# Performance work log

Measured on AMD Instinct MI355X. Metric: run time of the kernel, lower is better.

Reference implementation:

```python
import jax, jax.numpy as jnp
import numpy as np

B, L, V, H = 2, 2048, 1024, 16
HD = V // H  # head size 64
EPS = 1e-3   # keras LayerNormalization default


def setup_inputs() -> dict:
    key = jax.random.key(0)
    ks = jax.random.split(key, 10)
    scale = 1.0 / np.sqrt(V)
    return {
        "query": jax.random.normal(ks[0], (B, L, V), jnp.float32),
        "key_t": jax.random.normal(ks[1], (B, L, V), jnp.float32),
        "value": jax.random.normal(ks[2], (B, L, V), jnp.float32),
        "Wq": jax.random.normal(ks[3], (H, V, HD), jnp.float32) * scale,
        "Wk": jax.random.normal(ks[4], (H, V, HD), jnp.float32) * scale,
        "Wv": jax.random.normal(ks[5], (H, V, HD), jnp.float32) * scale,
        "gamma": jnp.ones((V,), jnp.float32),
        "beta": jnp.zeros((V,), jnp.float32),
        "query_mask": jax.random.randint(ks[6], (B, L), 0, 2, jnp.int32),
        "value_mask": jax.random.randint(ks[7], (B, L), 0, 2, jnp.int32),
    }


def reference(query, key_t, value, Wq, Wk, Wv, gamma, beta, query_mask, value_mask):
    qm = query_mask.astype(jnp.float32)  # (B,L)
    vm = value_mask.astype(jnp.float32)  # (B,L)

    # per-head no-bias Dense projections, batched over heads
    Q = jnp.einsum('blv,hvd->bhld', query, Wq)
    K = jnp.einsum('blv,hvd->bhld', key_t, Wk)
    Vh = jnp.einsum('blv,hvd->bhld', value, Wv)

    scores = jnp.einsum('bhld,bhmd->bhlm', Q, K) / jnp.sqrt(jnp.float32(HD))
    attn = jax.nn.softmax(scores, axis=-1)

    # post-softmax multiplicative masking (faithful to original)
    tri = jnp.tril(jnp.ones((L, L), jnp.float32))  # (L,L) causal
    attn = attn * tri[None, None, :, :]
    attn = attn * qm[:, None, :, None] * vm[:, None, None, :]

    heads = jnp.einsum('bhlm,bhmd->bhld', attn, Vh)
    x = heads.transpose(0, 2, 1, 3).reshape(B, L, V)  # concat heads

    # dropout is identity at inference
    y = x + query
    mu = jnp.mean(y, axis=-1, keepdims=True)
    var = jnp.mean((y - mu) ** 2, axis=-1, keepdims=True)
    return gamma * (y - mu) * jax.lax.rsqrt(var + EPS) + beta
```

## Files before the change

kernel.cpp:

```cpp
#include <hip/hip_runtime.h>
#include <math.h>

constexpr int NB = 2;
constexpr int SL = 2048;
constexpr int NV = 1024;
constexpr int NH = 16;
constexpr int DH = 64;
constexpr float LN_EPS = 1e-3f;

typedef __bf16 bf16_t;
typedef __bf16 v8bf __attribute__((ext_vector_type(8)));
typedef float  v4f  __attribute__((ext_vector_type(4)));

__device__ __forceinline__ unsigned pack_bf16(float a, float b) {
  unsigned short ua = __builtin_bit_cast(unsigned short, (bf16_t)a);
  unsigned short ub = __builtin_bit_cast(unsigned short, (bf16_t)b);
  return (unsigned)ua | ((unsigned)ub << 16);
}
__device__ __forceinline__ void async_cp16(const void* g, void* l) {
  __builtin_amdgcn_global_load_lds(
      (const __attribute__((address_space(1))) unsigned int*)g,
      (__attribute__((address_space(3))) unsigned int*)l, 16, 0, 0);
}
__device__ __forceinline__ void drain_dma() {
  asm volatile("s_waitcnt vmcnt(0)" ::: "memory");
}

__global__ __launch_bounds__(256)
void acvt(const float* __restrict__ q, const float* __restrict__ k,
          const float* __restrict__ v, bf16_t* __restrict__ oq,
          bf16_t* __restrict__ ok, bf16_t* __restrict__ ov) {
  const int z = blockIdx.y;
  const float* src = z == 0 ? q : (z == 1 ? k : v);
  bf16_t*      dst = z == 0 ? oq : (z == 1 ? ok : ov);
  const size_t i = ((size_t)blockIdx.x * 256 + threadIdx.x) * 4;
  float4 f = *(const float4*)(src + i);
  uint2 u = {pack_bf16(f.x, f.y), pack_bf16(f.z, f.w)};
  *(uint2*)(dst + i) = u;
}

__global__ __launch_bounds__(256)
void wcvt(const float* __restrict__ Wq, const float* __restrict__ Wk,
          const float* __restrict__ Wv, bf16_t* __restrict__ Wt) {
  __shared__ float ls[64][65];
  const int z = blockIdx.z;
  const float* W = z == 0 ? Wq : (z == 1 ? Wk : Wv);
  const float sc = z == 0 ? 0.125f * 1.44269504f : 1.0f;
  const int h = blockIdx.y, v0 = blockIdx.x * 64;
  const int t = threadIdx.x;
  const int rr = t >> 4, c4 = t & 15;
  const float* src = W + ((size_t)h * NV + v0) * DH;
#pragma unroll
  for (int it = 0; it < 4; ++it) {
    float4 f = *(const float4*)(src + (size_t)(rr + it * 16) * DH + c4 * 4);
    ls[rr + it * 16][c4 * 4 + 0] = f.x;
    ls[rr + it * 16][c4 * 4 + 1] = f.y;
    ls[rr + it * 16][c4 * 4 + 2] = f.z;
    ls[rr + it * 16][c4 * 4 + 3] = f.w;
  }
  __syncthreads();
  const int dd = t >> 2, vq = t & 3;
  bf16_t tmp[16];
#pragma unroll
  for (int i = 0; i < 16; ++i) tmp[i] = (bf16_t)(ls[vq * 16 + i][dd] * sc);
  bf16_t* dst = Wt + ((size_t)z * NV + h * 64 + dd) * NV + v0 + vq * 16;
  *(v8bf*)dst = *(v8bf*)&tmp[0];
  *(v8bf*)(dst + 8) = *(v8bf*)&tmp[8];
}

__global__ __launch_bounds__(256, 4)
void proj_mfma(const bf16_t* __restrict__ A0, const bf16_t* __restrict__ A1,
               const bf16_t* __restrict__ A2, const bf16_t* __restrict__ Wtb,
               const int* __restrict__ vmask,
               bf16_t* __restrict__ O0, bf16_t* __restrict__ O1,
               bf16_t* __restrict__ O2) {
  __shared__ __align__(16) bf16_t Asb[2][128 * 32];
  __shared__ __align__(16) bf16_t Wsb[2][128 * 32];

  const int z = blockIdx.z;
  const bf16_t* A   = z == 0 ? A0 : (z == 1 ? A1 : A2);
  bf16_t*       out = z == 0 ? O0 : (z == 1 ? O1 : O2);
  const bf16_t* W   = Wtb + (size_t)z * NV * NV;

  const int t = threadIdx.x, w = t >> 6, lane = t & 63;
  const int g = lane >> 4, lx = lane & 15;
  const int m0 = blockIdx.x * 128, n0 = blockIdx.y * 128;
  const int rbase = (w >> 1) * 64, cbase = (w & 1) * 64;

  const int sr = lane >> 2;
  const int sc = (lane & 3);
  auto stageA = [&](int k0, int buf) {
#pragma unroll
    for (int s = 0; s < 2; ++s) {
      const int r = w * 32 + s * 16 + sr;
      const int c = sc ^ (r & 3);
      async_cp16(A + (size_t)(m0 + r) * NV + k0 + c * 8,
                 (char*)Asb[buf] + (w * 32 + s * 16) * 64);
    }
  };
  auto stageW = [&](int k0, int buf) {
#pragma unroll
    for (int s = 0; s < 2; ++s) {
      const int r = w * 32 + s * 16 + sr;
      const int c = sc ^ (r & 3);
      async_cp16(W + (size_t)(n0 + r) * NV + k0 + c * 8,
                 (char*)Wsb[buf] + (w * 32 + s * 16) * 64);
    }
  };

  v4f acc[4][4] = {};
  stageA(0, 0);
  stageW(0, 0);

  for (int it = 0; it < 32; ++it) {
    const int buf = it & 1;
    drain_dma();
    __syncthreads();
    if (it < 31) {
      stageA((it + 1) * 32, buf ^ 1);
      stageW((it + 1) * 32, buf ^ 1);
    }
    v8bf af[4], wf[4];
#pragma unroll
    for (int rt = 0; rt < 4; ++rt) {
      const int row = rbase + rt * 16 + lx;
      af[rt] = *(const v8bf*)((const char*)Asb[buf] + row * 64 +
                              ((g ^ (row & 3)) * 16));
    }
#pragma unroll
    for (int ct = 0; ct < 4; ++ct) {
      const int row = cbase + ct * 16 + lx;
      wf[ct] = *(const v8bf*)((const char*)Wsb[buf] + row * 64 +
                              ((g ^ (row & 3)) * 16));
    }
#pragma unroll
    for (int rt = 0; rt < 4; ++rt)
#pragma unroll
      for (int ct = 0; ct < 4; ++ct)
        acc[rt][ct] = __builtin_amdgcn_mfma_f32_16x16x32_bf16(
            af[rt], wf[ct], acc[rt][ct], 0, 0, 0);
  }

  if (z < 2) {
#pragma unroll
    for (int rt = 0; rt < 4; ++rt) {
#pragma unroll
      for (int reg = 0; reg < 4; ++reg) {
        const int row = m0 + rbase + rt * 16 + g * 4 + reg;
        const int b = row >> 11, l = row & (SL - 1);
#pragma unroll
        for (int ct = 0; ct < 4; ++ct) {
          const int n = n0 + cbase + ct * 16 + lx;
          const int h = n >> 6, d = n & 63;
          out[((size_t)(b * NH + h) * SL + l) * DH + d] = (bf16_t)acc[rt][ct][reg];
        }
      }
    }
  } else {
#pragma unroll
    for (int rt = 0; rt < 4; ++rt) {
      const int row = m0 + rbase + rt * 16 + g * 4;
      const int b = row >> 11, l = row & (SL - 1);
      float vm0 = (float)vmask[b * SL + l + 0];
      float vm1 = (float)vmask[b * SL + l + 1];
      float vm2 = (float)vmask[b * SL + l + 2];
      float vm3 = (float)vmask[b * SL + l + 3];
#pragma unroll
      for (int ct = 0; ct < 4; ++ct) {
        const int n = n0 + cbase + ct * 16 + lx;
        const int h = n >> 6, d = n & 63;
        uint2 u = {pack_bf16(acc[rt][ct][0] * vm0, acc[rt][ct][1] * vm1),
                   pack_bf16(acc[rt][ct][2] * vm2, acc[rt][ct][3] * vm3)};
        *(uint2*)&out[((size_t)(b * NH + h) * DH + d) * SL + l] = u;
      }
    }
  }
}

__global__ __launch_bounds__(256, 4)
void attn_mfma(const bf16_t* __restrict__ Qg, const bf16_t* __restrict__ Kg,
               const bf16_t* __restrict__ Vtg_all, const int* __restrict__ qmask,
               float* __restrict__ Xout) {
  __shared__ __align__(16) bf16_t kbuf[2][64 * 64];
  __shared__ __align__(16) bf16_t vbuf[2][64 * 64];
  __shared__ __align__(16) bf16_t Ps[4][32 * 32];

  const int id = blockIdx.x;
  const int bh = (id & 7) | ((id >> 8) << 3);
  const int qraw = (id >> 3) & 31;
  const int qb = ((id >> 8) & 1) ? qraw : 31 - qraw;
  const int t = threadIdx.x, w = t >> 6, lane = t & 63;
  const int wq = w & 1, wm = w >> 1;
  const int g = lane >> 4, lx = lane & 15;
  const int b = bh >> 4, h = bh & 15;
  const int l0 = qb * 64;
  const int lastAct = qb;

  const bf16_t* Kb  = Kg + (size_t)bh * SL * DH;
  const bf16_t* Vtg = Vtg_all + (size_t)bh * DH * SL;

  v8bf qf[2][2];
#pragma unroll
  for (int qt = 0; qt < 2; ++qt)
#pragma unroll
    for (int ks = 0; ks < 2; ++ks)
      qf[qt][ks] = *(const v8bf*)&Qg[((size_t)bh * SL + l0 + wq * 32 + qt * 16 + lx) * DH +
                                     ks * 32 + g * 8];

  v4f O[2][4] = {};
  float suml[2] = {0.f, 0.f};

  const int sr_off = lane >> 3, sc_l = lane & 7;
  auto stageK = [&](int mb, int buf) {
#pragma unroll
    for (int s = 0; s < 2; ++s) {
      const int r = w * 16 + s * 8 + sr_off;
      const int c = sc_l ^ (r & 7);
      async_cp16(Kb + (size_t)(mb + r) * DH + c * 8,
                 (char*)kbuf[buf] + (w * 16 + s * 8) * 128);
    }
  };
  auto stageV = [&](int mb, int buf) {
#pragma unroll
    for (int s = 0; s < 2; ++s) {
      const int r = w * 16 + s * 8 + sr_off;
      const int c = sc_l ^ (r & 7);
      async_cp16(Vtg + (size_t)r * SL + mb + c * 8,
                 (char*)vbuf[buf] + (w * 16 + s * 8) * 128);
    }
  };

  stageK(0, 0);
  stageV(0, 0);

  for (int mt = 0; mt <= lastAct; ++mt) {
    const int pb = mt & 1;
    drain_dma();
    __syncthreads();
    if (mt < SL / 64 - 1)  stageK((mt + 1) * 64, pb ^ 1);
    if (mt + 1 <= lastAct) stageV((mt + 1) * 64, pb ^ 1);

    v4f S[2][2];
#pragma unroll
    for (int mt2 = 0; mt2 < 2; ++mt2) {
      S[mt2][0] = (v4f){0.f, 0.f, 0.f, 0.f};
      S[mt2][1] = (v4f){0.f, 0.f, 0.f, 0.f};
    }
#pragma unroll
    for (int ks = 0; ks < 2; ++ks)
#pragma unroll
      for (int mt2 = 0; mt2 < 2; ++mt2) {
        const int row = wm * 32 + mt2 * 16 + lx;
        v8bf kf = *(const v8bf*)((const char*)kbuf[pb] + row * 128 +
                                 (((ks * 4 + g) ^ (lx & 7)) * 16));
#pragma unroll
        for (int qt = 0; qt < 2; ++qt)
          S[mt2][qt] = __builtin_amdgcn_mfma_f32_16x16x32_bf16(
              kf, qf[qt][ks], S[mt2][qt], 0, 0, 0);
      }

    const bool diagzone = (mt == qb);
#pragma unroll
    for (int mt2 = 0; mt2 < 2; ++mt2)
#pragma unroll
      for (int qt = 0; qt < 2; ++qt) {
        float e0 = __builtin_amdgcn_exp2f(S[mt2][qt][0]);
        float e1 = __builtin_amdgcn_exp2f(S[mt2][qt][1]);
        float e2 = __builtin_amdgcn_exp2f(S[mt2][qt][2]);
        float e3 = __builtin_amdgcn_exp2f(S[mt2][qt][3]);
        suml[qt] += (e0 + e1) + (e2 + e3);
        if (diagzone) {
          const int ml = mt * 64 + wm * 32 + mt2 * 16 + g * 4;
          const int ql = l0 + wq * 32 + qt * 16 + lx;
          e0 = (ml + 0 <= ql) ? e0 : 0.f;
          e1 = (ml + 1 <= ql) ? e1 : 0.f;
          e2 = (ml + 2 <= ql) ? e2 : 0.f;
          e3 = (ml + 3 <= ql) ? e3 : 0.f;
        }
        uint2 u = {pack_bf16(e0, e1), pack_bf16(e2, e3)};
        *(uint2*)((char*)Ps[w] + (qt * 16 + lx) * 64 +
                  (((mt2 * 2 + (g >> 1)) ^ ((lx >> 1) & 3)) * 16) +
                  (g & 1) * 8) = u;
      }

    __builtin_amdgcn_wave_barrier();

    v8bf pf[2];
#pragma unroll
    for (int qt = 0; qt < 2; ++qt)
      pf[qt] = *(const v8bf*)((const char*)Ps[w] + (qt * 16 + lx) * 64 +
                              ((g ^ ((lx >> 1) & 3)) * 16));
#pragma unroll
    for (int dt = 0; dt < 4; ++dt) {
      const int row = dt * 16 + lx;
      v8bf vf = *(const v8bf*)((const char*)vbuf[pb] + row * 128 +
                               (((wm * 4 + g) ^ (lx & 7)) * 16));
#pragma unroll
      for (int qt = 0; qt < 2; ++qt)
        O[qt][dt] = __builtin_amdgcn_mfma_f32_16x16x32_bf16(
            pf[qt], vf, O[qt][dt], 0, 0, 0);
    }
  }

  for (int mt = lastAct + 1; mt < SL / 64; ++mt) {
    const int pb = mt & 1;
    drain_dma();
    __syncthreads();
    if (mt < SL / 64 - 1) stageK((mt + 1) * 64, pb ^ 1);
    v4f S[2][2];
#pragma unroll
    for (int mt2 = 0; mt2 < 2; ++mt2) {
      S[mt2][0] = (v4f){0.f, 0.f, 0.f, 0.f};
      S[mt2][1] = (v4f){0.f, 0.f, 0.f, 0.f};
    }
#pragma unroll
    for (int ks = 0; ks < 2; ++ks)
#pragma unroll
      for (int mt2 = 0; mt2 < 2; ++mt2) {
        const int row = wm * 32 + mt2 * 16 + lx;
        v8bf kf = *(const v8bf*)((const char*)kbuf[pb] + row * 128 +
                                 (((ks * 4 + g) ^ (lx & 7)) * 16));
#pragma unroll
        for (int qt = 0; qt < 2; ++qt)
          S[mt2][qt] = __builtin_amdgcn_mfma_f32_16x16x32_bf16(
              kf, qf[qt][ks], S[mt2][qt], 0, 0, 0);
      }
#pragma unroll
    for (int mt2 = 0; mt2 < 2; ++mt2)
#pragma unroll
      for (int qt = 0; qt < 2; ++qt)
        suml[qt] += (__builtin_amdgcn_exp2f(S[mt2][qt][0]) +
                     __builtin_amdgcn_exp2f(S[mt2][qt][1])) +
                    (__builtin_amdgcn_exp2f(S[mt2][qt][2]) +
                     __builtin_amdgcn_exp2f(S[mt2][qt][3]));
  }

  suml[0] += __shfl_xor(suml[0], 16); suml[0] += __shfl_xor(suml[0], 32);
  suml[1] += __shfl_xor(suml[1], 16); suml[1] += __shfl_xor(suml[1], 32);

  __syncthreads();
  float* obuf = (float*)&kbuf[0][0];
  float* sbuf = (float*)&vbuf[0][0];
  if (g == 0) {
    sbuf[((wq * 2 + wm) * 2 + 0) * 16 + lx] = suml[0];
    sbuf[((wq * 2 + wm) * 2 + 1) * 16 + lx] = suml[1];
  }
  if (wm == 1) {
#pragma unroll
    for (int qt = 0; qt < 2; ++qt)
#pragma unroll
      for (int dt = 0; dt < 4; ++dt)
#pragma unroll
        for (int reg = 0; reg < 4; ++reg)
          obuf[wq * 2048 + (qt * 16 + g * 4 + reg) * 64 +
               ((dt * 16 + lx) ^ ((g & 1) * 16))] = O[qt][dt][reg];
  }
  __syncthreads();
  if (wm == 0) {
#pragma unroll
    for (int qt = 0; qt < 2; ++qt) {
      const float stot = suml[qt] + sbuf[((wq * 2 + 1) * 2 + qt) * 16 + lx];
#pragma unroll
      for (int reg = 0; reg < 4; ++reg) {
        const int q = l0 + wq * 32 + qt * 16 + g * 4 + reg;
        const float den = __shfl(stot, g * 4 + reg);
        const float inv = (float)qmask[b * SL + q] / den;
#pragma unroll
        for (int dt = 0; dt < 4; ++dt) {
          const float val =
              (O[qt][dt][reg] +
               obuf[wq * 2048 + (qt * 16 + g * 4 + reg) * 64 +
                    ((dt * 16 + lx) ^ ((g & 1) * 16))]) *
              inv;
          Xout[((size_t)(b * SL + q)) * NV + h * DH + dt * 16 + lx] = val;
        }
      }
    }
  }
}

__global__ __launch_bounds__(256)
void ln_kernel(const float* __restrict__ X, const float* __restrict__ query,
               const float* __restrict__ gamma, const float* __restrict__ beta,
               float* __restrict__ out) {
  const int row = blockIdx.x * 4 + (threadIdx.x >> 6);
  const int lane = threadIdx.x & 63;
  const float* xr = X + (size_t)row * NV;
  const float* qr = query + (size_t)row * NV;
  float4 y[4];
  float s = 0.f, ss = 0.f;
#pragma unroll
  for (int i = 0; i < 4; ++i) {
    const int col = lane * 4 + i * 256;
    float4 xv = *(const float4*)(xr + col);
    float4 qv = *(const float4*)(qr + col);
    y[i].x = xv.x + qv.x; y[i].y = xv.y + qv.y;
    y[i].z = xv.z + qv.z; y[i].w = xv.w + qv.w;
    s  += (y[i].x + y[i].y) + (y[i].z + y[i].w);
    ss += (y[i].x * y[i].x + y[i].y * y[i].y) +
          (y[i].z * y[i].z + y[i].w * y[i].w);
  }
#pragma unroll
  for (int off = 1; off < 64; off <<= 1) {
    s  += __shfl_xor(s, off);
    ss += __shfl_xor(ss, off);
  }
  const float mu   = s * (1.f / NV);
  const float var  = ss * (1.f / NV) - mu * mu;
  const float rstd = rsqrtf(var + LN_EPS);
#pragma unroll
  for (int i = 0; i < 4; ++i) {
    const int col = lane * 4 + i * 256;
    float4 gv = *(const float4*)(gamma + col);
    float4 bv = *(const float4*)(beta + col);
    float4 o;
    o.x = gv.x * (y[i].x - mu) * rstd + bv.x;
    o.y = gv.y * (y[i].y - mu) * rstd + bv.y;
    o.z = gv.z * (y[i].z - mu) * rstd + bv.z;
    o.w = gv.w * (y[i].w - mu) * rstd + bv.w;
    *(float4*)(out + (size_t)row * NV + col) = o;
  }
}

extern "C" void kernel_launch(void* const* d_in, const int* in_sizes, int n_in,
                              void* d_out, int out_size, void* d_ws, size_t ws_size,
                              hipStream_t stream) {
  const float* query = (const float*)d_in[0];
  const float* key_t = (const float*)d_in[1];
  const float* value = (const float*)d_in[2];
  const float* Wq    = (const float*)d_in[3];
  const float* Wk    = (const float*)d_in[4];
  const float* Wv    = (const float*)d_in[5];
  const float* gamma = (const float*)d_in[6];
  const float* beta  = (const float*)d_in[7];
  const int*   qmask = (const int*)d_in[8];
  const int*   vmask = (const int*)d_in[9];
  float* out = (float*)d_out;

  const size_t per = (size_t)NB * NH * SL * DH;
  bf16_t* Qws = (bf16_t*)d_ws;
  bf16_t* Kws = Qws + per;
  bf16_t* Vws = Kws + per;
  bf16_t* Wtb = Vws + per;
  bf16_t* Aq  = Wtb + (size_t)3 * NV * NV;
  bf16_t* Ak  = Aq + per;
  bf16_t* Av  = Ak + per;

  acvt<<<dim3((NB * SL * NV) / (256 * 4), 3), 256, 0, stream>>>(
      query, key_t, value, Aq, Ak, Av);
  wcvt<<<dim3(16, 16, 3), 256, 0, stream>>>(Wq, Wk, Wv, Wtb);
  proj_mfma<<<dim3(32, 8, 3), 256, 0, stream>>>(Aq, Ak, Av, Wtb,
                                                vmask, Qws, Kws, Vws);
  attn_mfma<<<1024, 256, 0, stream>>>(Qws, Kws, Vws, qmask, out);
  ln_kernel<<<NB * SL / 4, 256, 0, stream>>>(out, query, gamma, beta, out);
}
```

Before: 206.1 us.

## Load K and V fragments directly from global memory instead of LDS staging

Removes the double-buffered async global-to-LDS staging of K and V tiles and the per-iteration drain and block barrier. Each wave now loads its MFMA K and V fragments straight from global memory, and the shared buffer shrinks to hold only the P tiles and the epilogue buffers. This cuts LDS use and synchronisation, which may allow more resident blocks, but it gives up cross-wave reuse of K/V tiles and the prefetch overlap. Global and L2 traffic rises, and load latency is now exposed directly in the inner loop.

```diff
diff --git a/kernel.cpp b/kernel.cpp
--- a/kernel.cpp
+++ b/kernel.cpp
@@ -181,9 +181,10 @@
 void attn_mfma(const bf16_t* __restrict__ Qg, const bf16_t* __restrict__ Kg,
                const bf16_t* __restrict__ Vtg_all, const int* __restrict__ qmask,
                float* __restrict__ Xout) {
-  __shared__ __align__(16) bf16_t kbuf[2][64 * 64];
-  __shared__ __align__(16) bf16_t vbuf[2][64 * 64];
-  __shared__ __align__(16) bf16_t Ps[4][32 * 32];
+  __shared__ __align__(16) char smem[16896];
+  bf16_t* Ps   = (bf16_t*)smem;
+  float*  obuf = (float*)smem;
+  float*  sbuf = (float*)(smem + 16384);
 
   const int id = blockIdx.x;
   const int bh = (id & 7) | ((id >> 8) << 3);
@@ -210,36 +211,8 @@
   v4f O[2][4] = {};
   float suml[2] = {0.f, 0.f};
 
-  const int sr_off = lane >> 3, sc_l = lane & 7;
-  auto stageK = [&](int mb, int buf) {
-#pragma unroll
-    for (int s = 0; s < 2; ++s) {
-      const int r = w * 16 + s * 8 + sr_off;
-      const int c = sc_l ^ (r & 7);
-      async_cp16(Kb + (size_t)(mb + r) * DH + c * 8,
-                 (char*)kbuf[buf] + (w * 16 + s * 8) * 128);
-    }
-  };
-  auto stageV = [&](int mb, int buf) {
-#pragma unroll
-    for (int s = 0; s < 2; ++s) {
-      const int r = w * 16 + s * 8 + sr_off;
-      const int c = sc_l ^ (r & 7);
-      async_cp16(Vtg + (size_t)r * SL + mb + c * 8,
-                 (char*)vbuf[buf] + (w * 16 + s * 8) * 128);
-    }
-  };
-
-  stageK(0, 0);
-  stageV(0, 0);
-
   for (int mt = 0; mt <= lastAct; ++mt) {
-    const int pb = mt & 1;
-    drain_dma();
-    __syncthreads();
-    if (mt < SL / 64 - 1)  stageK((mt + 1) * 64, pb ^ 1);
-    if (mt + 1 <= lastAct) stageV((mt + 1) * 64, pb ^ 1);
-
+    const int mb = mt * 64;
     v4f S[2][2];
 #pragma unroll
     for (int mt2 = 0; mt2 < 2; ++mt2) {
@@ -250,9 +223,8 @@
     for (int ks = 0; ks < 2; ++ks)
 #pragma unroll
       for (int mt2 = 0; mt2 < 2; ++mt2) {
-        const int row = wm * 32 + mt2 * 16 + lx;
-        v8bf kf = *(const v8bf*)((const char*)kbuf[pb] + row * 128 +
-                                 (((ks * 4 + g) ^ (lx & 7)) * 16));
+        v8bf kf = *(const v8bf*)&Kb[(size_t)(mb + wm * 32 + mt2 * 16 + lx) * DH +
+                                    ks * 32 + g * 8];
 #pragma unroll
         for (int qt = 0; qt < 2; ++qt)
           S[mt2][qt] = __builtin_amdgcn_mfma_f32_16x16x32_bf16(
@@ -270,7 +242,7 @@
         float e3 = __builtin_amdgcn_exp2f(S[mt2][qt][3]);
         suml[qt] += (e0 + e1) + (e2 + e3);
         if (diagzone) {
-          const int ml = mt * 64 + wm * 32 + mt2 * 16 + g * 4;
+          const int ml = mb + wm * 32 + mt2 * 16 + g * 4;
           const int ql = l0 + wq * 32 + qt * 16 + lx;
           e0 = (ml + 0 <= ql) ? e0 : 0.f;
           e1 = (ml + 1 <= ql) ? e1 : 0.f;
@@ -278,7 +250,7 @@
           e3 = (ml + 3 <= ql) ? e3 : 0.f;
         }
         uint2 u = {pack_bf16(e0, e1), pack_bf16(e2, e3)};
-        *(uint2*)((char*)Ps[w] + (qt * 16 + lx) * 64 +
+        *(uint2*)((char*)&Ps[w * 1024] + (qt * 16 + lx) * 64 +
                   (((mt2 * 2 + (g >> 1)) ^ ((lx >> 1) & 3)) * 16) +
                   (g & 1) * 8) = u;
       }
@@ -288,13 +260,12 @@
     v8bf pf[2];
 #pragma unroll
     for (int qt = 0; qt < 2; ++qt)
-      pf[qt] = *(const v8bf*)((const char*)Ps[w] + (qt * 16 + lx) * 64 +
+      pf[qt] = *(const v8bf*)((const char*)&Ps[w * 1024] + (qt * 16 + lx) * 64 +
                               ((g ^ ((lx >> 1) & 3)) * 16));
 #pragma unroll
     for (int dt = 0; dt < 4; ++dt) {
-      const int row = dt * 16 + lx;
-      v8bf vf = *(const v8bf*)((const char*)vbuf[pb] + row * 128 +
-                               (((wm * 4 + g) ^ (lx & 7)) * 16));
+      v8bf vf = *(const v8bf*)&Vtg[(size_t)(dt * 16 + lx) * SL + mb +
+                                   wm * 32 + g * 8];
 #pragma unroll
       for (int qt = 0; qt < 2; ++qt)
         O[qt][dt] = __builtin_amdgcn_mfma_f32_16x16x32_bf16(
@@ -303,10 +274,7 @@
   }
 
   for (int mt = lastAct + 1; mt < SL / 64; ++mt) {
-    const int pb = mt & 1;
-    drain_dma();
-    __syncthreads();
-    if (mt < SL / 64 - 1) stageK((mt + 1) * 64, pb ^ 1);
+    const int mb = mt * 64;
     v4f S[2][2];
 #pragma unroll
     for (int mt2 = 0; mt2 < 2; ++mt2) {
@@ -317,9 +285,8 @@
     for (int ks = 0; ks < 2; ++ks)
 #pragma unroll
       for (int mt2 = 0; mt2 < 2; ++mt2) {
-        const int row = wm * 32 + mt2 * 16 + lx;
-        v8bf kf = *(const v8bf*)((const char*)kbuf[pb] + row * 128 +
-                                 (((ks * 4 + g) ^ (lx & 7)) * 16));
+        v8bf kf = *(const v8bf*)&Kb[(size_t)(mb + wm * 32 + mt2 * 16 + lx) * DH +
+                                    ks * 32 + g * 8];
 #pragma unroll
         for (int qt = 0; qt < 2; ++qt)
           S[mt2][qt] = __builtin_amdgcn_mfma_f32_16x16x32_bf16(
@@ -339,8 +306,6 @@
   suml[1] += __shfl_xor(suml[1], 16); suml[1] += __shfl_xor(suml[1], 32);
 
   __syncthreads();
-  float* obuf = (float*)&kbuf[0][0];
-  float* sbuf = (float*)&vbuf[0][0];
   if (g == 0) {
     sbuf[((wq * 2 + wm) * 2 + 0) * 16 + lx] = suml[0];
     sbuf[((wq * 2 + wm) * 2 + 1) * 16 + lx] = suml[1];
```

After: 246.7 us. 19.7% more time.
